# Kernel optimization log

Measured on AMD Instinct MI355X. Metric: run time of the kernel, lower is better.

The kernel has to match this reference:

```python
import jax, jax.numpy as jnp
import numpy as np

K_SIZE, STRIDE, PAD = 3, 1, 1
B, C1, C2, H, W = 2, 256, 256, 64, 64


def conv2d(x, w, b, stride, pad):
    out = jax.lax.conv_general_dilated(
        x, w, (stride, stride), [(pad, pad), (pad, pad)],
        dimension_numbers=("NCHW", "OIHW", "NCHW"))
    return out + b[None, :, None, None]


def deform_conv2d(x, offset, mask, w, b, k, stride, pad):
    # torchvision.ops.deform_conv2d semantics (modulated, offset_groups=1)
    Bn, C, Hh, Ww = x.shape
    Ho, Wo = offset.shape[2], offset.shape[3]
    K = k * k
    # offset channels are (dy, dx) interleaved per kernel point
    off = offset.reshape(Bn, K, 2, Ho, Wo)
    dy, dx = off[:, :, 0], off[:, :, 1]          # [B,K,Ho,Wo]
    ki = jnp.arange(k)
    kyy, kxx = jnp.meshgrid(ki, ki, indexing="ij")
    kyy, kxx = kyy.reshape(K), kxx.reshape(K)
    base_y = (jnp.arange(Ho) * stride - pad)[None, :, None] + kyy[:, None, None]  # [K,Ho,1]
    base_x = (jnp.arange(Wo) * stride - pad)[None, None, :] + kxx[:, None, None]  # [K,1,Wo]
    ys = base_y[None].astype(x.dtype) + dy       # [B,K,Ho,Wo]
    xs = base_x[None].astype(x.dtype) + dx
    N = K * Ho * Wo
    ysf, xsf = ys.reshape(Bn, N), xs.reshape(Bn, N)
    y0 = jnp.floor(ysf)
    x0 = jnp.floor(xsf)
    ly, lx = ysf - y0, xsf - x0                  # bilinear fractions
    y0i, x0i = y0.astype(jnp.int32), x0.astype(jnp.int32)
    xf = x.reshape(Bn, C, Hh * Ww)

    def gather(yi, xi):
        valid = (yi >= 0) & (yi < Hh) & (xi >= 0) & (xi < Ww)
        idx = jnp.clip(yi, 0, Hh - 1) * Ww + jnp.clip(xi, 0, Ww - 1)
        v = jnp.take_along_axis(xf, idx[:, None, :], axis=2)  # [B,C,N]
        return v * valid[:, None, :].astype(x.dtype)

    v00 = gather(y0i, x0i)
    v01 = gather(y0i, x0i + 1)
    v10 = gather(y0i + 1, x0i)
    v11 = gather(y0i + 1, x0i + 1)
    wy1, wx1 = ly[:, None], lx[:, None]
    val = (v00 * (1 - wy1) * (1 - wx1) + v01 * (1 - wy1) * wx1 +
           v10 * wy1 * (1 - wx1) + v11 * wy1 * wx1)          # [B,C,N]
    val = val.reshape(Bn, C, K, Ho, Wo) * mask[:, None]       # modulate
    out = jnp.einsum("ock,bckhw->bohw", w.reshape(w.shape[0], C, K), val)
    return out + b[None, :, None, None]


def setup_inputs() -> dict:
    key = jax.random.key(0)
    ks = jax.random.split(key, 6)
    k2 = K_SIZE * K_SIZE
    return {
        "x": jax.random.normal(ks[0], (B, C1, H, W), jnp.float32),
        "offset_feat": jax.random.normal(ks[1], (B, C2, H, W), jnp.float32),
        # offset/mask head conv (zero-init in module; small random so offsets are non-trivial)
        "w_offset_mask": jax.random.normal(ks[2], (3 * k2, C2, K_SIZE, K_SIZE), jnp.float32) * 0.01,
        "b_offset_mask": jax.random.normal(ks[3], (3 * k2,), jnp.float32) * 0.01,
        "w_dcn": jax.random.normal(ks[4], (C2, C1, K_SIZE, K_SIZE), jnp.float32) / np.sqrt(C1 * k2),
        "b_dcn": jax.random.normal(ks[5], (C2,), jnp.float32) * 0.01,
    }


def reference(x, offset_feat, w_offset_mask, b_offset_mask, w_dcn, b_dcn):
    om = conv2d(offset_feat, w_offset_mask, b_offset_mask, STRIDE, PAD)  # [B,3*k*k,Ho,Wo]
    o1, o2, m = jnp.split(om, 3, axis=1)
    offset = jnp.concatenate([o1, o2], axis=1)   # [B,2*k*k,Ho,Wo]
    mask = jax.nn.sigmoid(m)                      # [B,k*k,Ho,Wo]
    return deform_conv2d(x, offset, mask, w_dcn, b_dcn, K_SIZE, STRIDE, PAD)
```

## Files before the change

### kernel.cpp

```cpp
#include <hip/hip_runtime.h>
#include <math.h>

#define BATCH 2
#define CIN   256
#define COUT  256
#define COFF  256
#define HWPIX 4096
#define CKTOT 2304
#define VSTR  40
#define PH    66
#define PHW   4356
#define NKG   12

typedef __attribute__((ext_vector_type(8))) short short8;
typedef __attribute__((ext_vector_type(8))) unsigned short ushort8;
typedef __attribute__((ext_vector_type(4))) float float4v;

__device__ __forceinline__ unsigned short f2bf(float f) {
    unsigned u = __float_as_uint(f);
    unsigned r = (u + 0x7FFFu + ((u >> 16) & 1u)) >> 16;
    return (unsigned short)r;
}
__device__ __forceinline__ float bf2f(unsigned short h) {
    return __uint_as_float(((unsigned)h) << 16);
}

__global__ __launch_bounds__(256) void prep_kernel(
    const float* __restrict__ x, const float* __restrict__ feat,
    const float* __restrict__ wdcn, const float* __restrict__ wom,
    unsigned short* __restrict__ xTh,
    unsigned short* __restrict__ fh,
    unsigned short* __restrict__ whi,
    unsigned short* __restrict__ wohi)
{
    const int bid = blockIdx.x;
    const int tid = threadIdx.x;

    if (bid < 4096) {
        const bool isx = bid < 2048;
        const int lb = isx ? bid : bid - 2048;
        const int b  = lb >> 10;
        const int r  = lb & 1023;
        const int pt = r >> 3;
        const int ct = r & 7;
        __shared__ float t[32][33];
        const int tx = tid & 31, ty = tid >> 5;
        const float* src = isx ? x : feat;
        const float* sb = src + ((size_t)b * 256 + ct * 32) * HWPIX + pt * 32;
#pragma unroll
        for (int i = ty; i < 32; i += 8)
            t[i][tx] = sb[(size_t)i * HWPIX + tx];
        __syncthreads();
        if (isx) {
            unsigned short* ob = xTh + ((size_t)b * HWPIX + pt * 32) * 256 + ct * 32;
#pragma unroll
            for (int i = ty; i < 32; i += 8)
                ob[(size_t)i * 256 + tx] = f2bf(t[tx][i]);
        } else {
#pragma unroll
            for (int i = ty; i < 32; i += 8) {
                int p = pt * 32 + i;
                int row = (p >> 6) + 1, col = (p & 63) + 1;
                fh[((size_t)b * PHW + row * PH + col) * 256 + ct * 32 + tx]
                    = f2bf(t[tx][i]);
            }
        }
    } else if (bid < 6400) {
        int gid = (bid - 4096) * 256 + tid;
        int cc  = gid & 31;
        int co  = (gid >> 5) & 255;
        int kcb = gid >> 13;
        int k   = kcb >> 3;
        int cb  = kcb & 7;
        float w = wdcn[((size_t)co * 256 + cb * 32 + cc) * 9 + k];
        whi[gid] = f2bf(w);
    } else if (bid < 6688) {
        int gid = (bid - 6400) * 256 + tid;
        int cc  = gid & 31;
        int co  = (gid >> 5) & 31;
        int kcb = gid >> 10;
        int k   = kcb >> 3;
        int cb  = kcb & 7;
        float w = 0.0f;
        if (co < 27) w = wom[(size_t)co * CKTOT + (cb * 32 + cc) * 9 + k];
        wohi[gid] = f2bf(w);
    } else {
        int idx = (bid - 6688) * 256 + tid;
        int b = idx / 66560;
        int r = idx - b * 66560;
        int pidx = r >> 8;
        int c = r & 255;
        int row, col;
        if (pidx < 66)       { row = 0;           col = pidx; }
        else if (pidx < 132) { row = 65;          col = pidx - 66; }
        else if (pidx < 196) { row = pidx - 131;  col = 0; }
        else                 { row = pidx - 195;  col = 65; }
        fh[((size_t)b * PHW + row * PH + col) * 256 + c] = 0;
    }
}

__global__ __launch_bounds__(256) void conv_om_mfma_kernel(
    const unsigned short* __restrict__ fh,
    const unsigned short* __restrict__ wohi,
    float* __restrict__ om12)
{
    const int y  = blockIdx.x;
    const int kg = blockIdx.y;
    const int b  = blockIdx.z;
    const int tid = threadIdx.x;
    const int wv  = tid >> 6;
    const int lane = tid & 63;
    const int l15 = lane & 15;
    const int q   = lane >> 4;
    const int xg  = wv * 16 + l15;

    float4v acc[2];
    acc[0] = (float4v)0.0f;
    acc[1] = (float4v)0.0f;

    const unsigned short* fhb = fh + (size_t)b * PHW * 256;

#pragma unroll 3
    for (int i = 0; i < 6; ++i) {
        int kcb = kg * 6 + i;
        int k  = kcb >> 3;
        int cb = kcb & 7;
        size_t s = ((size_t)((y + k / 3) * PH + xg + k % 3)) * 256 + cb * 32 + q * 8;
        short8 bh = *(const short8*)(fhb + s);
        short8 ah0 = *(const short8*)(wohi + ((size_t)kcb * 32 + l15) * 32 + q * 8);
        short8 ah1 = *(const short8*)(wohi + ((size_t)kcb * 32 + 16 + l15) * 32 + q * 8);
        acc[0] = __builtin_amdgcn_mfma_f32_16x16x32_bf16(ah0, bh, acc[0], 0, 0, 0);
        acc[1] = __builtin_amdgcn_mfma_f32_16x16x32_bf16(ah1, bh, acc[1], 0, 0, 0);
    }

    const int p = y * 64 + xg;
    float* ob = om12 + (size_t)(kg * 2 + b) * 27 * HWPIX;
#pragma unroll
    for (int t = 0; t < 2; ++t) {
#pragma unroll
        for (int r = 0; r < 4; ++r) {
            int co = t * 16 + q * 4 + r;
            if (co < 27) ob[co * HWPIX + p] = acc[t][r];
        }
    }
}

__global__ __launch_bounds__(256) void dcn_mfma_kernel(
    const unsigned short* __restrict__ xTh,
    const float* __restrict__ om12,
    const unsigned short* __restrict__ whi,
    const float* __restrict__ bom,
    const float* __restrict__ bdcn,
    float* __restrict__ out)
{
    const int tid = threadIdx.x;
    const int y   = blockIdx.x >> 1;
    const int xh  = blockIdx.x & 1;
    const int cog = blockIdx.y;
    const int b   = blockIdx.z;

    __shared__ float4 s_wt[288];
    __shared__ int4   s_ix[288];
    __shared__ unsigned short V[288 * VSTR];

    for (int idx = tid; idx < 288; idx += 256) {
        int k   = idx >> 5;
        int pxl = idx & 31;
        int xg  = xh * 32 + pxl;
        int p   = y * 64 + xg;
        float dy = bom[2 * k], dx = bom[2 * k + 1], mm = bom[18 + k];
#pragma unroll
        for (int g = 0; g < NKG; ++g) {
            const float* ob = om12 + (size_t)(g * 2 + b) * 27 * HWPIX;
            dy += ob[(2 * k) * HWPIX + p];
            dx += ob[(2 * k + 1) * HWPIX + p];
            mm += ob[(18 + k) * HWPIX + p];
        }
        float ys = (float)(y  - 1 + (k / 3)) + dy;
        float xs = (float)(xg - 1 + (k % 3)) + dx;
        float y0f = floorf(ys), x0f = floorf(xs);
        int y0 = (int)y0f, x0 = (int)x0f;
        float ly = ys - y0f, lx = xs - x0f;
        float m  = 1.0f / (1.0f + expf(-mm));
        bool yv0 = ((unsigned)y0 < 64u), yv1 = ((unsigned)(y0 + 1) < 64u);
        bool xv0 = ((unsigned)x0 < 64u), xv1 = ((unsigned)(x0 + 1) < 64u);
        int i00 = y0 * 64 + x0;
        float4 wt;
        int4 ix;
        wt.x = (yv0 && xv0) ? (1.0f - ly) * (1.0f - lx) * m : 0.0f;
        wt.y = (yv0 && xv1) ? (1.0f - ly) * lx * m          : 0.0f;
        wt.z = (yv1 && xv0) ? ly * (1.0f - lx) * m          : 0.0f;
        wt.w = (yv1 && xv1) ? ly * lx * m                   : 0.0f;
        ix.x = (yv0 && xv0) ? i00      : 0;
        ix.y = (yv0 && xv1) ? i00 + 1  : 0;
        ix.z = (yv1 && xv0) ? i00 + 64 : 0;
        ix.w = (yv1 && xv1) ? i00 + 65 : 0;
        s_wt[idx] = wt;
        s_ix[idx] = ix;
    }
    __syncthreads();

    const int w    = tid >> 6;
    const int lane = tid & 63;
    const int l15  = lane & 15;
    const int q    = lane >> 4;

    const int cg   = tid & 3;
    const int spx  = (tid >> 2) & 31;
    const int tapg = tid >> 7;

    float4v acc[2][2];
#pragma unroll
    for (int t = 0; t < 2; ++t)
#pragma unroll
        for (int p = 0; p < 2; ++p) acc[t][p] = (float4v)0.0f;

    const unsigned short* xb = xTh + ((size_t)b << 12) * 256;

    for (int cb = 0; cb < 8; ++cb) {
        {
            const unsigned short* xc = xb + cb * 32 + cg * 8;
#pragma unroll 3
            for (int j = 0; j < 5; ++j) {
                int k = 2 * j + tapg;
                if (k > 8) break;
                int cidx = k * 32 + spx;
                float4 wt = s_wt[cidx];
                int4   ix = s_ix[cidx];
                ushort8 u00 = *(const ushort8*)(xc + (size_t)ix.x * 256);
                ushort8 u01 = *(const ushort8*)(xc + (size_t)ix.y * 256);
                ushort8 u10 = *(const ushort8*)(xc + (size_t)ix.z * 256);
                ushort8 u11 = *(const ushort8*)(xc + (size_t)ix.w * 256);
                unsigned hv[4];
#pragma unroll
                for (int jj = 0; jj < 4; ++jj) {
                    float va = wt.x * bf2f(u00[2 * jj])     + wt.y * bf2f(u01[2 * jj])
                             + wt.z * bf2f(u10[2 * jj])     + wt.w * bf2f(u11[2 * jj]);
                    float vb = wt.x * bf2f(u00[2 * jj + 1]) + wt.y * bf2f(u01[2 * jj + 1])
                             + wt.z * bf2f(u10[2 * jj + 1]) + wt.w * bf2f(u11[2 * jj + 1]);
                    hv[jj] = (unsigned)f2bf(va) | ((unsigned)f2bf(vb) << 16);
                }
                *(uint4*)&V[cidx * VSTR + cg * 8]
                    = make_uint4(hv[0], hv[1], hv[2], hv[3]);
            }
        }
        __syncthreads();

#pragma unroll 3
        for (int k = 0; k < 9; ++k) {
            const int kcb = k * 8 + cb;
            size_t base = ((size_t)kcb * 256 + cog * 128 + w * 32 + l15) * 32 + q * 8;
            short8 ah0 = *(const short8*)(whi + base);
            short8 ah1 = *(const short8*)(whi + base + 16 * 32);
            short8 bh0 = *(const short8*)&V[(k * 32 + l15) * VSTR + q * 8];
            short8 bh1 = *(const short8*)&V[(k * 32 + 16 + l15) * VSTR + q * 8];
            acc[0][0] = __builtin_amdgcn_mfma_f32_16x16x32_bf16(ah0, bh0, acc[0][0], 0, 0, 0);
            acc[0][1] = __builtin_amdgcn_mfma_f32_16x16x32_bf16(ah0, bh1, acc[0][1], 0, 0, 0);
            acc[1][0] = __builtin_amdgcn_mfma_f32_16x16x32_bf16(ah1, bh0, acc[1][0], 0, 0, 0);
            acc[1][1] = __builtin_amdgcn_mfma_f32_16x16x32_bf16(ah1, bh1, acc[1][1], 0, 0, 0);
        }
        __syncthreads();
    }

#pragma unroll
    for (int t = 0; t < 2; ++t) {
#pragma unroll
        for (int r = 0; r < 4; ++r) {
            int co = cog * 128 + w * 32 + t * 16 + q * 4 + r;
            float bias = bdcn[co];
#pragma unroll
            for (int p = 0; p < 2; ++p) {
                int px = xh * 32 + p * 16 + l15;
                out[(((size_t)b * COUT + co) << 12) + y * 64 + px]
                    = acc[t][p][r] + bias;
            }
        }
    }
}

extern "C" void kernel_launch(void* const* d_in, const int* in_sizes, int n_in,
                              void* d_out, int out_size, void* d_ws, size_t ws_size,
                              hipStream_t stream)
{
    const float* x    = (const float*)d_in[0];
    const float* feat = (const float*)d_in[1];
    const float* wom  = (const float*)d_in[2];
    const float* bom  = (const float*)d_in[3];
    const float* wdcn = (const float*)d_in[4];
    const float* bdcn = (const float*)d_in[5];
    float* out = (float*)d_out;

    float* om12          = (float*)d_ws;
    unsigned short* whi  = (unsigned short*)(om12 + (size_t)NKG * 2 * 27 * HWPIX);
    unsigned short* wohi = whi + (size_t)CKTOT * 256;
    unsigned short* xTh  = wohi + 73728;
    unsigned short* fh   = xTh + (size_t)2 * HWPIX * 256;

    prep_kernel<<<7208, 256, 0, stream>>>(x, feat, wdcn, wom, xTh, fh,
                                          whi, wohi);

    dim3 gco(64, NKG, 2);
    conv_om_mfma_kernel<<<gco, 256, 0, stream>>>(fh, wohi, om12);

    dim3 grid(128, 2, 2);
    dcn_mfma_kernel<<<grid, 256, 0, stream>>>(xTh, om12, whi, bom, bdcn, out);
}
```

Measured before the change: 133.6 us.

## Split deformable conv into separate sampling kernel and global-memory GEMM kernel

Result: slower. 221.7 us (+66.0%).

```diff
diff --git a/kernel.cpp b/kernel.cpp
--- a/kernel.cpp
+++ b/kernel.cpp
@@ -4,13 +4,11 @@
 #define BATCH 2
 #define CIN   256
 #define COUT  256
-#define COFF  256
 #define HWPIX 4096
 #define CKTOT 2304
-#define VSTR  40
 #define PH    66
 #define PHW   4356
-#define NKG   12
+#define NKG   8
 
 typedef __attribute__((ext_vector_type(8))) short short8;
 typedef __attribute__((ext_vector_type(8))) unsigned short ushort8;
@@ -102,7 +100,7 @@
 __global__ __launch_bounds__(256) void conv_om_mfma_kernel(
     const unsigned short* __restrict__ fh,
     const unsigned short* __restrict__ wohi,
-    float* __restrict__ om12)
+    float* __restrict__ om8)
 {
     const int y  = blockIdx.x;
     const int kg = blockIdx.y;
@@ -121,8 +119,8 @@
     const unsigned short* fhb = fh + (size_t)b * PHW * 256;
 
 #pragma unroll 3
-    for (int i = 0; i < 6; ++i) {
-        int kcb = kg * 6 + i;
+    for (int i = 0; i < 9; ++i) {
+        int kcb = kg * 9 + i;
         int k  = kcb >> 3;
         int cb = kcb & 7;
         size_t s = ((size_t)((y + k / 3) * PH + xg + k % 3)) * 256 + cb * 32 + q * 8;
@@ -134,7 +132,7 @@
     }
 
     const int p = y * 64 + xg;
-    float* ob = om12 + (size_t)(kg * 2 + b) * 27 * HWPIX;
+    float* ob = om8 + (size_t)(kg * 2 + b) * 27 * HWPIX;
 #pragma unroll
     for (int t = 0; t < 2; ++t) {
 #pragma unroll
@@ -145,135 +143,110 @@
     }
 }
 
-__global__ __launch_bounds__(256) void dcn_mfma_kernel(
+__global__ __launch_bounds__(256) void sample_kernel(
     const unsigned short* __restrict__ xTh,
-    const float* __restrict__ om12,
+    const float* __restrict__ om8,
+    const float* __restrict__ bom,
+    unsigned short* __restrict__ V,
+    int b)
+{
+    const int tid = threadIdx.x;
+    const int k   = blockIdx.y;
+    const int px  = blockIdx.x * 64 + (tid >> 2);
+    const int cpart = tid & 3;
+    const int y  = px >> 6, xg = px & 63;
+
+    float dy = bom[2 * k], dx = bom[2 * k + 1], mm = bom[18 + k];
+#pragma unroll
+    for (int g = 0; g < NKG; ++g) {
+        const float* ob = om8 + (size_t)(g * 2 + b) * 27 * HWPIX;
+        dy += ob[(2 * k) * HWPIX + px];
+        dx += ob[(2 * k + 1) * HWPIX + px];
+        mm += ob[(18 + k) * HWPIX + px];
+    }
+    float ys = (float)(y  - 1 + (k / 3)) + dy;
+    float xs = (float)(xg - 1 + (k % 3)) + dx;
+    float y0f = floorf(ys), x0f = floorf(xs);
+    int y0 = (int)y0f, x0 = (int)x0f;
+    float ly = ys - y0f, lx = xs - x0f;
+    float m  = 1.0f / (1.0f + expf(-mm));
+    bool yv0 = ((unsigned)y0 < 64u), yv1 = ((unsigned)(y0 + 1) < 64u);
+    bool xv0 = ((unsigned)x0 < 64u), xv1 = ((unsigned)(x0 + 1) < 64u);
+    int i00 = y0 * 64 + x0;
+    float w00 = (yv0 && xv0) ? (1.0f - ly) * (1.0f - lx) * m : 0.0f;
+    float w01 = (yv0 && xv1) ? (1.0f - ly) * lx * m          : 0.0f;
+    float w10 = (yv1 && xv0) ? ly * (1.0f - lx) * m          : 0.0f;
+    float w11 = (yv1 && xv1) ? ly * lx * m                   : 0.0f;
+    int j00 = (yv0 && xv0) ? i00      : 0;
+    int j01 = (yv0 && xv1) ? i00 + 1  : 0;
+    int j10 = (yv1 && xv0) ? i00 + 64 : 0;
+    int j11 = (yv1 && xv1) ? i00 + 65 : 0;
+
+    const unsigned short* xc = xTh + ((size_t)b << 12) * 256 + cpart * 64;
+
+#pragma unroll 2
+    for (int j = 0; j < 8; ++j) {
+        int c0 = cpart * 64 + j * 8;
+        ushort8 u00 = *(const ushort8*)(xc + (size_t)j00 * 256 + j * 8);
+        ushort8 u01 = *(const ushort8*)(xc + (size_t)j01 * 256 + j * 8);
+        ushort8 u10 = *(const ushort8*)(xc + (size_t)j10 * 256 + j * 8);
+        ushort8 u11 = *(const ushort8*)(xc + (size_t)j11 * 256 + j * 8);
+        unsigned hv[4];
+#pragma unroll
+        for (int jj = 0; jj < 4; ++jj) {
+            float va = w00 * bf2f(u00[2 * jj])     + w01 * bf2f(u01[2 * jj])
+                     + w10 * bf2f(u10[2 * jj])     + w11 * bf2f(u11[2 * jj]);
+            float vb = w00 * bf2f(u00[2 * jj + 1]) + w01 * bf2f(u01[2 * jj + 1])
+                     + w10 * bf2f(u10[2 * jj + 1]) + w11 * bf2f(u11[2 * jj + 1]);
+            hv[jj] = (unsigned)f2bf(va) | ((unsigned)f2bf(vb) << 16);
+        }
+        int cb = c0 >> 5, cc = c0 & 31;
+        int kcb = k * 8 + cb;
+        *(uint4*)&V[((size_t)kcb * HWPIX + px) * 32 + cc]
+            = make_uint4(hv[0], hv[1], hv[2], hv[3]);
+    }
+}
+
+__global__ __launch_bounds__(256) void gemm_kernel(
+    const unsigned short* __restrict__ V,
     const unsigned short* __restrict__ whi,
-    const float* __restrict__ bom,
     const float* __restrict__ bdcn,
-    float* __restrict__ out)
-{
-    const int tid = threadIdx.x;
-    const int y   = blockIdx.x >> 1;
-    const int xh  = blockIdx.x & 1;
-    const int cog = blockIdx.y;
-    const int b   = blockIdx.z;
-
-    __shared__ float4 s_wt[288];
-    __shared__ int4   s_ix[288];
-    __shared__ unsigned short V[288 * VSTR];
-
-    for (int idx = tid; idx < 288; idx += 256) {
-        int k   = idx >> 5;
-        int pxl = idx & 31;
-        int xg  = xh * 32 + pxl;
-        int p   = y * 64 + xg;
-        float dy = bom[2 * k], dx = bom[2 * k + 1], mm = bom[18 + k];
-#pragma unroll
-        for (int g = 0; g < NKG; ++g) {
-            const float* ob = om12 + (size_t)(g * 2 + b) * 27 * HWPIX;
-            dy += ob[(2 * k) * HWPIX + p];
-            dx += ob[(2 * k + 1) * HWPIX + p];
-            mm += ob[(18 + k) * HWPIX + p];
-        }
-        float ys = (float)(y  - 1 + (k / 3)) + dy;
-        float xs = (float)(xg - 1 + (k % 3)) + dx;
-        float y0f = floorf(ys), x0f = floorf(xs);
-        int y0 = (int)y0f, x0 = (int)x0f;
-        float ly = ys - y0f, lx = xs - x0f;
-        float m  = 1.0f / (1.0f + expf(-mm));
-        bool yv0 = ((unsigned)y0 < 64u), yv1 = ((unsigned)(y0 + 1) < 64u);
-        bool xv0 = ((unsigned)x0 < 64u), xv1 = ((unsigned)(x0 + 1) < 64u);
-        int i00 = y0 * 64 + x0;
-        float4 wt;
-        int4 ix;
-        wt.x = (yv0 && xv0) ? (1.0f - ly) * (1.0f - lx) * m : 0.0f;
-        wt.y = (yv0 && xv1) ? (1.0f - ly) * lx * m          : 0.0f;
-        wt.z = (yv1 && xv0) ? ly * (1.0f - lx) * m          : 0.0f;
-        wt.w = (yv1 && xv1) ? ly * lx * m                   : 0.0f;
-        ix.x = (yv0 && xv0) ? i00      : 0;
-        ix.y = (yv0 && xv1) ? i00 + 1  : 0;
-        ix.z = (yv1 && xv0) ? i00 + 64 : 0;
-        ix.w = (yv1 && xv1) ? i00 + 65 : 0;
-        s_wt[idx] = wt;
-        s_ix[idx] = ix;
-    }
-    __syncthreads();
-
-    const int w    = tid >> 6;
+    float* __restrict__ out,
+    int b)
+{
+    const int tid = threadIdx.x;
+    const int coT = blockIdx.x;
+    const int pxT = blockIdx.y;
+    const int w   = tid >> 6;
     const int lane = tid & 63;
-    const int l15  = lane & 15;
-    const int q    = lane >> 4;
-
-    const int cg   = tid & 3;
-    const int spx  = (tid >> 2) & 31;
-    const int tapg = tid >> 7;
-
-    float4v acc[2][2];
-#pragma unroll
-    for (int t = 0; t < 2; ++t)
-#pragma unroll
-        for (int p = 0; p < 2; ++p) acc[t][p] = (float4v)0.0f;
-
-    const unsigned short* xb = xTh + ((size_t)b << 12) * 256;
-
-    for (int cb = 0; cb < 8; ++cb) {
-        {
-            const unsigned short* xc = xb + cb * 32 + cg * 8;
+    const int l15 = lane & 15;
+    const int q   = lane >> 4;
+    const int px0 = pxT * 64 + w * 16;
+
+    float4v acc[4];
+#pragma unroll
+    for (int t = 0; t < 4; ++t) acc[t] = (float4v)0.0f;
+
 #pragma unroll 3
-            for (int j = 0; j < 5; ++j) {
-                int k = 2 * j + tapg;
-                if (k > 8) break;
-                int cidx = k * 32 + spx;
-                float4 wt = s_wt[cidx];
-                int4   ix = s_ix[cidx];
-                ushort8 u00 = *(const ushort8*)(xc + (size_t)ix.x * 256);
-                ushort8 u01 = *(const ushort8*)(xc + (size_t)ix.y * 256);
-                ushort8 u10 = *(const ushort8*)(xc + (size_t)ix.z * 256);
-                ushort8 u11 = *(const ushort8*)(xc + (size_t)ix.w * 256);
-                unsigned hv[4];
-#pragma unroll
-                for (int jj = 0; jj < 4; ++jj) {
-                    float va = wt.x * bf2f(u00[2 * jj])     + wt.y * bf2f(u01[2 * jj])
-                             + wt.z * bf2f(u10[2 * jj])     + wt.w * bf2f(u11[2 * jj]);
-                    float vb = wt.x * bf2f(u00[2 * jj + 1]) + wt.y * bf2f(u01[2 * jj + 1])
-                             + wt.z * bf2f(u10[2 * jj + 1]) + wt.w * bf2f(u11[2 * jj + 1]);
-                    hv[jj] = (unsigned)f2bf(va) | ((unsigned)f2bf(vb) << 16);
-                }
-                *(uint4*)&V[cidx * VSTR + cg * 8]
-                    = make_uint4(hv[0], hv[1], hv[2], hv[3]);
-            }
-        }
-        __syncthreads();
-
-#pragma unroll 3
-        for (int k = 0; k < 9; ++k) {
-            const int kcb = k * 8 + cb;
-            size_t base = ((size_t)kcb * 256 + cog * 128 + w * 32 + l15) * 32 + q * 8;
-            short8 ah0 = *(const short8*)(whi + base);
-            short8 ah1 = *(const short8*)(whi + base + 16 * 32);
-            short8 bh0 = *(const short8*)&V[(k * 32 + l15) * VSTR + q * 8];
-            short8 bh1 = *(const short8*)&V[(k * 32 + 16 + l15) * VSTR + q * 8];
-            acc[0][0] = __builtin_amdgcn_mfma_f32_16x16x32_bf16(ah0, bh0, acc[0][0], 0, 0, 0);
-            acc[0][1] = __builtin_amdgcn_mfma_f32_16x16x32_bf16(ah0, bh1, acc[0][1], 0, 0, 0);
-            acc[1][0] = __builtin_amdgcn_mfma_f32_16x16x32_bf16(ah1, bh0, acc[1][0], 0, 0, 0);
-            acc[1][1] = __builtin_amdgcn_mfma_f32_16x16x32_bf16(ah1, bh1, acc[1][1], 0, 0, 0);
-        }
-        __syncthreads();
-    }
-
-#pragma unroll
-    for (int t = 0; t < 2; ++t) {
+    for (int kcb = 0; kcb < 72; ++kcb) {
+        short8 bf = *(const short8*)(V + ((size_t)kcb * HWPIX + px0 + l15) * 32 + q * 8);
+        size_t ab = ((size_t)kcb * 256 + coT * 64 + l15) * 32 + q * 8;
+        short8 a0 = *(const short8*)(whi + ab);
+        short8 a1 = *(const short8*)(whi + ab + 16 * 32);
+        short8 a2 = *(const short8*)(whi + ab + 32 * 32);
+        short8 a3 = *(const short8*)(whi + ab + 48 * 32);
+        acc[0] = __builtin_amdgcn_mfma_f32_16x16x32_bf16(a0, bf, acc[0], 0, 0, 0);
+        acc[1] = __builtin_amdgcn_mfma_f32_16x16x32_bf16(a1, bf, acc[1], 0, 0, 0);
+        acc[2] = __builtin_amdgcn_mfma_f32_16x16x32_bf16(a2, bf, acc[2], 0, 0, 0);
+        acc[3] = __builtin_amdgcn_mfma_f32_16x16x32_bf16(a3, bf, acc[3], 0, 0, 0);
+    }
+
+#pragma unroll
+    for (int t = 0; t < 4; ++t) {
 #pragma unroll
         for (int r = 0; r < 4; ++r) {
-            int co = cog * 128 + w * 32 + t * 16 + q * 4 + r;
-            float bias = bdcn[co];
-#pragma unroll
-            for (int p = 0; p < 2; ++p) {
-                int px = xh * 32 + p * 16 + l15;
-                out[(((size_t)b * COUT + co) << 12) + y * 64 + px]
-                    = acc[t][p][r] + bias;
-            }
+            int co = coT * 64 + t * 16 + q * 4 + r;
+            out[(((size_t)b * COUT + co) << 12) + px0 + l15] = acc[t][r] + bdcn[co];
         }
     }
 }
@@ -290,18 +263,23 @@
     const float* bdcn = (const float*)d_in[5];
     float* out = (float*)d_out;
 
-    float* om12          = (float*)d_ws;
-    unsigned short* whi  = (unsigned short*)(om12 + (size_t)NKG * 2 * 27 * HWPIX);
+    float* om8           = (float*)d_ws;
+    unsigned short* whi  = (unsigned short*)(om8 + (size_t)NKG * 2 * 27 * HWPIX);
     unsigned short* wohi = whi + (size_t)CKTOT * 256;
     unsigned short* xTh  = wohi + 73728;
     unsigned short* fh   = xTh + (size_t)2 * HWPIX * 256;
+    unsigned short* V    = fh + (size_t)2 * PHW * 256;
 
     prep_kernel<<<7208, 256, 0, stream>>>(x, feat, wdcn, wom, xTh, fh,
                                           whi, wohi);
 
     dim3 gco(64, NKG, 2);
-    conv_om_mfma_kernel<<<gco, 256, 0, stream>>>(fh, wohi, om12);
-
-    dim3 grid(128, 2, 2);
-    dcn_mfma_kernel<<<grid, 256, 0, stream>>>(xTh, om12, whi, bom, bdcn, out);
-}
+    conv_om_mfma_kernel<<<gco, 256, 0, stream>>>(fh, wohi, om8);
+
+    for (int b = 0; b < 2; ++b) {
+        dim3 gs(64, 9);
+        sample_kernel<<<gs, 256, 0, stream>>>(xTh, om8, bom, V, b);
+        dim3 gg(4, 64);
+        gemm_kernel<<<gg, 256, 0, stream>>>(V, whi, bdcn, out, b);
+    }
+}
```

## Double-buffer the bilinear-sampled V tile to overlap gather with MFMA

Applied to the files above, without the earlier changes.

Measured after the change: 133.9 us. Within noise of the previous version (+0.3%).

```diff
diff --git a/kernel.cpp b/kernel.cpp
--- a/kernel.cpp
+++ b/kernel.cpp
@@ -8,6 +8,7 @@
 #define HWPIX 4096
 #define CKTOT 2304
 #define VSTR  40
+#define VSLOT (288 * VSTR)
 #define PH    66
 #define PHW   4356
 #define NKG   12
@@ -161,7 +162,7 @@
 
     __shared__ float4 s_wt[288];
     __shared__ int4   s_ix[288];
-    __shared__ unsigned short V[288 * VSTR];
+    __shared__ unsigned short V[2 * VSLOT];
 
     for (int idx = tid; idx < 288; idx += 256) {
         int k   = idx >> 5;
@@ -217,9 +218,39 @@
 
     const unsigned short* xb = xTh + ((size_t)b << 12) * 256;
 
+    {
+        const unsigned short* xc = xb + 0 * 32 + cg * 8;
+#pragma unroll 3
+        for (int j = 0; j < 5; ++j) {
+            int k = 2 * j + tapg;
+            if (k > 8) break;
+            int cidx = k * 32 + spx;
+            float4 wt = s_wt[cidx];
+            int4   ix = s_ix[cidx];
+            ushort8 u00 = *(const ushort8*)(xc + (size_t)ix.x * 256);
+            ushort8 u01 = *(const ushort8*)(xc + (size_t)ix.y * 256);
+            ushort8 u10 = *(const ushort8*)(xc + (size_t)ix.z * 256);
+            ushort8 u11 = *(const ushort8*)(xc + (size_t)ix.w * 256);
+            unsigned hv[4];
+#pragma unroll
+            for (int jj = 0; jj < 4; ++jj) {
+                float va = wt.x * bf2f(u00[2 * jj])     + wt.y * bf2f(u01[2 * jj])
+                         + wt.z * bf2f(u10[2 * jj])     + wt.w * bf2f(u11[2 * jj]);
+                float vb = wt.x * bf2f(u00[2 * jj + 1]) + wt.y * bf2f(u01[2 * jj + 1])
+                         + wt.z * bf2f(u10[2 * jj + 1]) + wt.w * bf2f(u11[2 * jj + 1]);
+                hv[jj] = (unsigned)f2bf(va) | ((unsigned)f2bf(vb) << 16);
+            }
+            *(uint4*)&V[cidx * VSTR + cg * 8] = make_uint4(hv[0], hv[1], hv[2], hv[3]);
+        }
+    }
+    __syncthreads();
+
     for (int cb = 0; cb < 8; ++cb) {
-        {
-            const unsigned short* xc = xb + cb * 32 + cg * 8;
+        const unsigned short* Vc = V + (cb & 1) * VSLOT;
+
+        if (cb < 7) {
+            unsigned short* Vd = V + ((cb + 1) & 1) * VSLOT;
+            const unsigned short* xc = xb + (cb + 1) * 32 + cg * 8;
 #pragma unroll 3
             for (int j = 0; j < 5; ++j) {
                 int k = 2 * j + tapg;
@@ -240,11 +271,9 @@
                              + wt.z * bf2f(u10[2 * jj + 1]) + wt.w * bf2f(u11[2 * jj + 1]);
                     hv[jj] = (unsigned)f2bf(va) | ((unsigned)f2bf(vb) << 16);
                 }
-                *(uint4*)&V[cidx * VSTR + cg * 8]
-                    = make_uint4(hv[0], hv[1], hv[2], hv[3]);
+                *(uint4*)&Vd[cidx * VSTR + cg * 8] = make_uint4(hv[0], hv[1], hv[2], hv[3]);
             }
         }
-        __syncthreads();
 
 #pragma unroll 3
         for (int k = 0; k < 9; ++k) {
@@ -252,8 +281,8 @@
             size_t base = ((size_t)kcb * 256 + cog * 128 + w * 32 + l15) * 32 + q * 8;
             short8 ah0 = *(const short8*)(whi + base);
             short8 ah1 = *(const short8*)(whi + base + 16 * 32);
-            short8 bh0 = *(const short8*)&V[(k * 32 + l15) * VSTR + q * 8];
-            short8 bh1 = *(const short8*)&V[(k * 32 + 16 + l15) * VSTR + q * 8];
+            short8 bh0 = *(const short8*)&Vc[(k * 32 + l15) * VSTR + q * 8];
+            short8 bh1 = *(const short8*)&Vc[(k * 32 + 16 + l15) * VSTR + q * 8];
             acc[0][0] = __builtin_amdgcn_mfma_f32_16x16x32_bf16(ah0, bh0, acc[0][0], 0, 0, 0);
             acc[0][1] = __builtin_amdgcn_mfma_f32_16x16x32_bf16(ah0, bh1, acc[0][1], 0, 0, 0);
             acc[1][0] = __builtin_amdgcn_mfma_f32_16x16x32_bf16(ah1, bh0, acc[1][0], 0, 0, 0);
```
